# Kernel optimization log

Measured on AMD Instinct MI355X. Metric: run time of the kernel, lower is better.

## Reference

```python
import jax, jax.numpy as jnp
import numpy as np

KERNEL = 3
STRIDE = 1
PADDING = 1


def setup_inputs() -> dict:
    key = jax.random.key(0)
    k1, k2, k3 = jax.random.split(key, 3)
    x = jax.random.normal(k1, (8, 64, 128, 128), dtype=jnp.float32)
    # AdderLayer weight [O, C, kH, kW] and bias [O]
    w = jax.random.normal(k2, (64, 64, KERNEL, KERNEL), dtype=jnp.float32) * 0.1
    b = jax.random.normal(k3, (64,), dtype=jnp.float32)
    return {"x": x, "w": w, "b": b}


def _adder_conv_relu(x, w, b):
    # AdderNet conv: out[n,o,h,w] = -sum_{c,kh,kw} |x_patch - w[o]| (+ bias), then ReLU.
    N, C, H, W = x.shape
    O = w.shape[0]
    k = w.shape[2]
    # Extract patches: [N, C*k*k, Ho, Wo] (C is the slowest-varying feature dim,
    # matching w.reshape(O, -1) ordering)
    patches = jax.lax.conv_general_dilated_patches(
        x, (k, k), (STRIDE, STRIDE), [(PADDING, PADDING), (PADDING, PADDING)])
    Ho, Wo = patches.shape[2], patches.shape[3]
    P = patches.transpose(0, 2, 3, 1).reshape(-1, C * k * k)  # [N*Ho*Wo, Ckk]
    wf = w.reshape(O, -1)  # [O, Ckk]

    @jax.checkpoint
    def per_out(wb):
        wrow, bi = wb  # [Ckk], scalar
        # negative L1 distance + bias, fused with ReLU
        return jax.nn.relu(bi - jnp.abs(P - wrow[None, :]).sum(-1))  # [N*Ho*Wo]

    out = jax.lax.map(per_out, (wf, b))  # [O, N*Ho*Wo]
    return out.reshape(O, N, Ho, Wo).transpose(1, 0, 2, 3)  # [N, O, Ho, Wo]


def reference(x, w, b):
    return _adder_conv_relu(x, w, b)
```

## Files before the change

### kernel.cpp

```cpp
#include <hip/hip_runtime.h>

typedef unsigned int u32;


#define Hh 128
#define Ww 128
#define C_IN 64
#define O_OUT 64
#define NB 8
#define PIX (Hh * Ww)
#define CSUB 32

__global__ __launch_bounds__(256)
void adder_row_screen(const float* __restrict__ x, const float* __restrict__ w,
                      const float* __restrict__ b, float* __restrict__ out) {
    __shared__ float Ap[8 * 128];
    __shared__ float Afin[128];
    __shared__ float wmax[4];
    __shared__ u32   nfail;
    __shared__ u32   flist[128];

    const int tid = threadIdx.x;
    const int bid = blockIdx.x;
    const int n   = bid >> 7;
    const int h   = bid & 127;

    if (tid == 0) nfail = 0;

    const int c4 = tid & 31;
    const int g  = tid >> 5;
    const float4* xn = (const float4*)x + (size_t)n * C_IN * (PIX / 4)
                     + (size_t)h * (Ww / 4) + c4;
    float4 xv[4];
    #pragma unroll
    for (int k = 0; k < 4; ++k)
        xv[k] = xn[(size_t)(g + (k << 3)) * (PIX / 4)];

    float4* outn = (float4*)out + (size_t)n * O_OUT * (PIX / 4);
    const float4 z = make_float4(0.f, 0.f, 0.f, 0.f);
    #pragma unroll
    for (int j = 0; j < 8; ++j) {
        const int idx = (j << 8) + tid;
        const int o = idx >> 5, cc = idx & 31;
        outn[(size_t)o * (PIX / 4) + h * (Ww / 4) + cc] = z;
    }

    {
        const int o = tid >> 2, jj = tid & 3;
        float s = 0.f;
        #pragma unroll
        for (int c8 = 0; c8 < 8; ++c8) {
            const float* wp = w + (size_t)o * 576 + (jj * 8 + c8) * 9 + 3;
            s += fabsf(wp[0]) + fabsf(wp[1]) + fabsf(wp[2]);
        }
        s += __shfl_xor(s, 1); s += __shfl_xor(s, 2);
        float v = s + b[o];
        #pragma unroll
        for (int d = 4; d < 64; d <<= 1) v = fmaxf(v, __shfl_xor(v, d));
        if ((tid & 63) == 0) wmax[tid >> 6] = v;
    }

    {
        float4 a = make_float4(0.f, 0.f, 0.f, 0.f);
        #pragma unroll
        for (int k = 0; k < 4; ++k) {
            a.x += fabsf(xv[k].x); a.y += fabsf(xv[k].y);
            a.z += fabsf(xv[k].z); a.w += fabsf(xv[k].w);
        }
        *(float4*)&Ap[g * 128 + c4 * 4] = a;
    }
    __syncthreads();

    if (tid < 128) {
        float s = 0.f;
        #pragma unroll
        for (int gg = 0; gg < 8; ++gg) s += Ap[gg * 128 + tid];
        Afin[tid] = s;
    }
    __syncthreads();

    const float thr = fmaxf(fmaxf(wmax[0], wmax[1]),
                            fmaxf(wmax[2], wmax[3])) + 1.0f;

    if (tid < 128) {
        float S = Afin[tid];
        if (tid > 0)   S += Afin[tid - 1];
        if (tid < 127) S += Afin[tid + 1];
        if (!(S >= thr)) {
            u32 k = atomicAdd(&nfail, 1u);
            flist[k] = (u32)tid;
        }
    }
    __syncthreads();

    const u32 nf = nfail;
    if (nf) {
        const float* xs = x + (size_t)n * C_IN * PIX;
        for (u32 i = tid; i < nf * 64u; i += 256u) {
            const int col = (int)flist[i >> 6];
            const int o   = (int)(i & 63u);
            const float* wo = w + (size_t)o * C_IN * 9;
            float sum = 0.f;
            for (int c = 0; c < C_IN; ++c) {
                const float* xc = xs + (size_t)c * PIX;
                const float* wc = wo + c * 9;
                #pragma unroll
                for (int kh = 0; kh < 3; ++kh) {
                    const int gh = h + kh - 1;
                    #pragma unroll
                    for (int kw = 0; kw < 3; ++kw) {
                        const int gw = col + kw - 1;
                        const float xval = ((unsigned)gh < (unsigned)Hh &&
                                            (unsigned)gw < (unsigned)Ww)
                                           ? xc[gh * Ww + gw] : 0.f;
                        sum += fabsf(xval - wc[kh * 3 + kw]);
                    }
                }
            }
            out[(size_t)(n * O_OUT + o) * PIX + h * Ww + col] = fmaxf(b[o] - sum, 0.f);
        }
    }
}

extern "C" void kernel_launch(void* const* d_in, const int* in_sizes, int n_in,
                              void* d_out, int out_size, void* d_ws, size_t ws_size,
                              hipStream_t stream) {
    const float* x = (const float*)d_in[0];
    const float* w = (const float*)d_in[1];
    const float* b = (const float*)d_in[2];
    float* out = (float*)d_out;

    adder_row_screen<<<NB * Hh, 256, 0, stream>>>(x, w, b, out);
}
```

Measured before the change: 14.67 us.

## Split zero-fill and screening from exact fixup into two kernels via bitmask

The single fused kernel becomes two. The first interleaves zero-fill blocks with screening blocks; the screening blocks use a weaker bound built from 16 channels instead of 32 and write a per-row 128-bit fail mask with ballot. A second kernel of 8 blocks reads the masks and computes the exact adder-conv only for flagged pixels, one thread per 64-column half-row. This cuts the x reads and shared-memory atomics in the screen, but adds a second launch and a very serial fixup path that would be slow if many pixels fail the weaker bound.

```diff
diff --git a/kernel.cpp b/kernel.cpp
--- a/kernel.cpp
+++ b/kernel.cpp
@@ -1,6 +1,7 @@
 #include <hip/hip_runtime.h>
 
 typedef unsigned int u32;
+typedef unsigned long long u64;
 
 
 #define Hh 128
@@ -9,7 +10,116 @@
 #define O_OUT 64
 #define NB 8
 #define PIX (Hh * Ww)
-#define CSUB 32
+#define MASK_BYTES ((size_t)NB * Hh * 2 * 8)
+
+__global__ __launch_bounds__(256)
+void k1_fill_screen(const float* __restrict__ x, const float* __restrict__ w,
+                    const float* __restrict__ b, float* __restrict__ out,
+                    u64* __restrict__ mask) {
+    const int tid = threadIdx.x, bid = blockIdx.x;
+
+    if (!(bid & 1)) {
+        const int f = bid >> 1;
+        float4* o4 = (float4*)out + (size_t)f * 2048;
+        const float4 z = make_float4(0.f, 0.f, 0.f, 0.f);
+        #pragma unroll
+        for (int j = 0; j < 8; ++j) o4[(j << 8) + tid] = z;
+        return;
+    }
+
+    __shared__ float Ap[8 * 128];
+    __shared__ float Afin[128];
+    __shared__ float wmax[4];
+
+    const int s = bid >> 1;
+    const int n = s >> 7, h = s & 127;
+    const int c4 = tid & 31;
+    const int g  = tid >> 5;
+
+    const float4* xn = (const float4*)x + (size_t)n * C_IN * (PIX / 4)
+                     + (size_t)h * (Ww / 4) + c4;
+    const float4 a0 = xn[(size_t)g * (PIX / 4)];
+    const float4 a1 = xn[(size_t)(g + 8) * (PIX / 4)];
+
+    const int o = tid >> 2, jj = tid & 3;
+    float sthr = 0.f;
+    #pragma unroll
+    for (int k = 0; k < 4; ++k) {
+        const float* wp = w + (size_t)o * 576 + (jj * 4 + k) * 9 + 3;
+        sthr += fabsf(wp[0]) + fabsf(wp[1]) + fabsf(wp[2]);
+    }
+    sthr += __shfl_xor(sthr, 1); sthr += __shfl_xor(sthr, 2);
+    float v = sthr + b[o];
+    #pragma unroll
+    for (int d = 4; d < 64; d <<= 1) v = fmaxf(v, __shfl_xor(v, d));
+    if ((tid & 63) == 0) wmax[tid >> 6] = v;
+
+    float4 a;
+    a.x = fabsf(a0.x) + fabsf(a1.x); a.y = fabsf(a0.y) + fabsf(a1.y);
+    a.z = fabsf(a0.z) + fabsf(a1.z); a.w = fabsf(a0.w) + fabsf(a1.w);
+    *(float4*)&Ap[g * 128 + c4 * 4] = a;
+    __syncthreads();
+
+    if (tid < 128) {
+        float sum = 0.f;
+        #pragma unroll
+        for (int gg = 0; gg < 8; ++gg) sum += Ap[gg * 128 + tid];
+        Afin[tid] = sum;
+    }
+    __syncthreads();
+
+    const float thr = fmaxf(fmaxf(wmax[0], wmax[1]),
+                            fmaxf(wmax[2], wmax[3])) + 1.0f;
+
+    bool fail = false;
+    if (tid < 128) {
+        float S = Afin[tid];
+        if (tid > 0)   S += Afin[tid - 1];
+        if (tid < 127) S += Afin[tid + 1];
+        fail = !(S >= thr);
+    }
+    const u64 m = __ballot(fail);
+    if (tid < 128 && (tid & 63) == 0)
+        mask[(size_t)(n * Hh + h) * 2 + (tid >> 6)] = m;
+}
+
+__global__ __launch_bounds__(256)
+void k2_fixup(const float* __restrict__ x, const float* __restrict__ w,
+              const float* __restrict__ b, float* __restrict__ out,
+              const u64* __restrict__ mask) {
+    const int n = blockIdx.x, tid = threadIdx.x;
+    const u64 m = mask[(size_t)n * 256 + tid];
+    if (!m) return;
+    const int h = tid >> 1, cbase = (tid & 1) << 6;
+    const float* xs = x + (size_t)n * C_IN * PIX;
+    u64 mm = m;
+    while (mm) {
+        const int bit = __ffsll((unsigned long long)mm) - 1;
+        mm &= mm - 1;
+        const int col = cbase + bit;
+        for (int o = 0; o < O_OUT; ++o) {
+            const float* wo = w + (size_t)o * C_IN * 9;
+            float sum = 0.f;
+            for (int c = 0; c < C_IN; ++c) {
+                const float* xc = xs + (size_t)c * PIX;
+                const float* wc = wo + c * 9;
+                #pragma unroll
+                for (int kh = 0; kh < 3; ++kh) {
+                    const int gh = h + kh - 1;
+                    #pragma unroll
+                    for (int kw = 0; kw < 3; ++kw) {
+                        const int gw = col + kw - 1;
+                        const float xval = ((unsigned)gh < (unsigned)Hh &&
+                                            (unsigned)gw < (unsigned)Ww)
+                                           ? xc[gh * Ww + gw] : 0.f;
+                        sum += fabsf(xval - wc[kh * 3 + kw]);
+                    }
+                }
+            }
+            out[(size_t)(n * O_OUT + o) * PIX + h * Ww + col] = fmaxf(b[o] - sum, 0.f);
+        }
+    }
+}
 
 __global__ __launch_bounds__(256)
 void adder_row_screen(const float* __restrict__ x, const float* __restrict__ w,
@@ -24,7 +134,6 @@
     const int bid = blockIdx.x;
     const int n   = bid >> 7;
     const int h   = bid & 127;
-
     if (tid == 0) nfail = 0;
 
     const int c4 = tid & 31;
@@ -59,7 +168,6 @@
         for (int d = 4; d < 64; d <<= 1) v = fmaxf(v, __shfl_xor(v, d));
         if ((tid & 63) == 0) wmax[tid >> 6] = v;
     }
-
     {
         float4 a = make_float4(0.f, 0.f, 0.f, 0.f);
         #pragma unroll
@@ -70,7 +178,6 @@
         *(float4*)&Ap[g * 128 + c4 * 4] = a;
     }
     __syncthreads();
-
     if (tid < 128) {
         float s = 0.f;
         #pragma unroll
@@ -78,10 +185,8 @@
         Afin[tid] = s;
     }
     __syncthreads();
-
     const float thr = fmaxf(fmaxf(wmax[0], wmax[1]),
                             fmaxf(wmax[2], wmax[3])) + 1.0f;
-
     if (tid < 128) {
         float S = Afin[tid];
         if (tid > 0)   S += Afin[tid - 1];
@@ -92,7 +197,6 @@
         }
     }
     __syncthreads();
-
     const u32 nf = nfail;
     if (nf) {
         const float* xs = x + (size_t)n * C_IN * PIX;
@@ -130,5 +234,11 @@
     const float* b = (const float*)d_in[2];
     float* out = (float*)d_out;
 
-    adder_row_screen<<<NB * Hh, 256, 0, stream>>>(x, w, b, out);
-}
+    if (ws_size >= MASK_BYTES) {
+        u64* mask = (u64*)d_ws;
+        k1_fill_screen<<<2048, 256, 0, stream>>>(x, w, b, out, mask);
+        k2_fixup<<<NB, 256, 0, stream>>>(x, w, b, out, mask);
+    } else {
+        adder_row_screen<<<NB * Hh, 256, 0, stream>>>(x, w, b, out);
+    }
+}
```

Result: slower. 15.46 us (+5.3%).
